# Kernel optimization log

Hardware: AMD Instinct MI355X
Metric: run time of the kernel (lower is better)

Reference implementation:

```python
import jax, jax.numpy as jnp
import numpy as np

B, IN_DIM = 1024, 128
MBD_IN, MBD_OUT, MBD_K = 64, 50, 5
BN_EPS = 1e-5


def setup_inputs() -> dict:
    key = jax.random.key(0)
    ks = jax.random.split(key, 16)
    n = lambda k, s: jax.random.normal(k, s, dtype=jnp.float32)
    return {
        "x": n(ks[0], (B, IN_DIM)),
        # MLP: 128->256->128(BN)->64, LeakyReLU(0.2)
        "W1": n(ks[1], (IN_DIM, 256)) * 0.05, "b1": jnp.zeros((256,), jnp.float32),
        "W2": n(ks[2], (256, 128)) * 0.05, "b2": jnp.zeros((128,), jnp.float32),
        "gamma": jnp.ones((128,), jnp.float32), "beta": jnp.zeros((128,), jnp.float32),
        "W3": n(ks[3], (128, 64)) * 0.05, "b3": jnp.zeros((64,), jnp.float32),
        # SelfAttention1D(64, heads=1) on a length-1 token: softmax over a single
        # key is identically 1, so output = residual + out_proj(value_proj(h)).
        # Wq/Wk provably do not affect the output and are omitted.
        "Wv": n(ks[4], (64, 64)) * 0.05, "bv": jnp.zeros((64,), jnp.float32),
        "Wo": n(ks[5], (64, 64)) * 0.05, "bo": jnp.zeros((64,), jnp.float32),
        # MinibatchDiscrimination tensor T: [64, 50, 5], init 0.05*randn as in source
        "T": n(ks[6], (MBD_IN, MBD_OUT, MBD_K)) * 0.05,
        "Ws": n(ks[7], (MBD_IN + MBD_OUT, 1)) * 0.05, "bs": jnp.zeros((1,), jnp.float32),
    }


def _lrelu(h):
    return jnp.where(h > 0, h, 0.2 * h)


def reference(x, W1, b1, W2, b2, gamma, beta, W3, b3, Wv, bv, Wo, bo, T, Ws, bs):
    # --- MLP backbone (BatchNorm1d in training mode: batch statistics) ---
    h = _lrelu(x @ W1 + b1)                      # [B,256]
    h = h @ W2 + b2                              # [B,128]
    mu = h.mean(axis=0)
    var = ((h - mu) ** 2).mean(axis=0)           # biased variance (torch BN)
    h = (h - mu) * jax.lax.rsqrt(var + BN_EPS) * gamma + beta
    h = _lrelu(h)
    h = _lrelu(h @ W3 + b3)                      # [B,64]
    # --- SelfAttention1D, seq_len=1 -> attn weights == 1 ---
    h = h + (h @ Wv + bv) @ Wo + bo              # [B,64]
    # --- Minibatch discrimination: fused all-pairs L1 + exp-sum ---
    M = (h @ T.reshape(MBD_IN, MBD_OUT * MBD_K)).reshape(-1, MBD_OUT, MBD_K)  # [B,50,5]
    diff = jnp.abs(M[:, None, :, :] - M[None, :, :, :]).sum(-1)               # [B,B,50]
    o = jnp.exp(-diff).sum(axis=0) - 1.0          # [B,50] (self term exp(0)=1 removed)
    feat = jnp.concatenate([h, o], axis=1)        # [B,114]
    score = (feat @ Ws + bs).squeeze(-1)          # [B]
    return score
```

## Files before the change

kernel.cpp:

```cpp
#include <hip/hip_runtime.h>
#include <math.h>

#define LRELU(v) ((v) > 0.f ? (v) : 0.2f * (v))


__global__ __launch_bounds__(256) void k1_mlp12(
    const float* __restrict__ x,
    const float* __restrict__ W1, const float* __restrict__ b1,
    const float* __restrict__ W2, const float* __restrict__ b2,
    float* __restrict__ h2g, float* __restrict__ stats)
{
    __shared__ float xs[256];
    __shared__ float h1s[512];
    __shared__ float ssum[256];
    __shared__ float ssq[256];
    const int t = threadIdx.x;
    const int r0 = blockIdx.x * 2;

    xs[t] = x[r0 * 128 + t];
    __syncthreads();
    {
        float a0 = b1[t], a1 = a0;
        for (int k = 0; k < 128; ++k) {
            float w = W1[k * 256 + t];
            a0 += xs[k] * w;
            a1 += xs[128 + k] * w;
        }
        h1s[t] = LRELU(a0);
        h1s[256 + t] = LRELU(a1);
    }
    __syncthreads();
    {
        const int c = t & 127;
        const int rr = t >> 7;
        float a = b2[c];
        for (int k = 0; k < 256; ++k)
            a += h1s[rr * 256 + k] * W2[k * 128 + c];
        h2g[(r0 + rr) * 128 + c] = a;
        ssum[t] = a;
        ssq[t] = a * a;
    }
    __syncthreads();
    if (t < 128)      atomicAdd(stats + t, ssum[t] + ssum[128 + t]);
    else { int c = t - 128; atomicAdd(stats + 128 + c, ssq[c] + ssq[128 + c]); }
}

__global__ __launch_bounds__(256) void k2_bn_attn_m(
    const float* __restrict__ h2g, const float* __restrict__ stats,
    const float* __restrict__ gamma, const float* __restrict__ beta,
    const float* __restrict__ W3, const float* __restrict__ b3,
    const float* __restrict__ Wv, const float* __restrict__ bv,
    const float* __restrict__ Wo, const float* __restrict__ bo,
    const float* __restrict__ T2,
    float* __restrict__ h4g, float* __restrict__ Mt)
{
    __shared__ float a[256];
    __shared__ float h3s[128];
    __shared__ float vss[128];
    __shared__ float h4s[128];
    const int t = threadIdx.x;
    const int r0 = blockIdx.x * 2;
    {
        const int c = t & 127;
        float s = stats[c], ss = stats[128 + c];
        float mean = s * (1.f / 1024.f);
        float var = ss * (1.f / 1024.f) - mean * mean;
        float rstd = rsqrtf(var + 1e-5f);
        float v = (h2g[r0 * 128 + t] - mean) * rstd * gamma[c] + beta[c];
        a[t] = LRELU(v);
    }
    __syncthreads();
    const int row = t >> 6, col = t & 63;
    if (t < 128) {
        float acc = b3[col];
        for (int k = 0; k < 128; ++k) acc += a[row * 128 + k] * W3[k * 64 + col];
        h3s[row * 64 + col] = LRELU(acc);
    }
    __syncthreads();
    if (t < 128) {
        float acc = bv[col];
        for (int k = 0; k < 64; ++k) acc += h3s[row * 64 + k] * Wv[k * 64 + col];
        vss[row * 64 + col] = acc;
    }
    __syncthreads();
    if (t < 128) {
        float acc = bo[col];
        for (int k = 0; k < 64; ++k) acc += vss[row * 64 + k] * Wo[k * 64 + col];
        float h4 = h3s[row * 64 + col] + acc;
        h4s[row * 64 + col] = h4;
        h4g[(r0 + row) * 64 + col] = h4;
    }
    __syncthreads();
    if (t < 250) {
        float m0 = 0.f, m1 = 0.f;
        for (int k = 0; k < 64; ++k) {
            float w = T2[k * 250 + t];
            m0 += h4s[k] * w;
            m1 += h4s[64 + k] * w;
        }
        Mt[(size_t)t * 1024 + r0]     = m0;
        Mt[(size_t)t * 1024 + r0 + 1] = m1;
    } else {
        Mt[(size_t)t * 1024 + r0]     = 0.f;
        Mt[(size_t)t * 1024 + r0 + 1] = 0.f;
    }
    if (t < 4) {
        Mt[(size_t)(256 + t) * 1024 + r0]     = 0.f;
        Mt[(size_t)(256 + t) * 1024 + r0 + 1] = 0.f;
    }
}

__global__ __launch_bounds__(256) void k3_pairs(
    const float* __restrict__ Mt, float* __restrict__ opart)
{
    __shared__ float mi[2560];
    const int t = threadIdx.x;
    const int b = blockIdx.x;
    const int jt = b / 104;
    const int rem = b - jt * 104;
    const int ct = rem >> 3;
    const int ic = rem & 7;
    const int jl = t & 63, cl = t >> 6;
    const int j = jt * 64 + jl;
    const int c = ct * 4 + cl;
    const int i0 = ic * 128;

    for (int qq = 0; qq < 10; ++qq) {
        int idx = qq * 256 + t;
        int cc = idx >> 7, il = idx & 127;
        mi[idx] = Mt[(size_t)(ct * 20 + cc) * 1024 + i0 + il];
    }
    float mj0 = Mt[(size_t)(c * 5 + 0) * 1024 + j];
    float mj1 = Mt[(size_t)(c * 5 + 1) * 1024 + j];
    float mj2 = Mt[(size_t)(c * 5 + 2) * 1024 + j];
    float mj3 = Mt[(size_t)(c * 5 + 3) * 1024 + j];
    float mj4 = Mt[(size_t)(c * 5 + 4) * 1024 + j];
    __syncthreads();

    const float4* m0 = (const float4*)(mi + (cl * 5 + 0) * 128);
    const float4* m1 = (const float4*)(mi + (cl * 5 + 1) * 128);
    const float4* m2 = (const float4*)(mi + (cl * 5 + 2) * 128);
    const float4* m3 = (const float4*)(mi + (cl * 5 + 3) * 128);
    const float4* m4 = (const float4*)(mi + (cl * 5 + 4) * 128);

    float acc0 = 0.f, acc1 = 0.f, acc2 = 0.f, acc3 = 0.f;
    for (int q = 0; q < 32; ++q) {
        float4 v0 = m0[q], v1 = m1[q], v2 = m2[q], v3 = m3[q], v4 = m4[q];
        float d0 = fabsf(v0.x - mj0) + fabsf(v1.x - mj1) + fabsf(v2.x - mj2)
                 + fabsf(v3.x - mj3) + fabsf(v4.x - mj4);
        float d1 = fabsf(v0.y - mj0) + fabsf(v1.y - mj1) + fabsf(v2.y - mj2)
                 + fabsf(v3.y - mj3) + fabsf(v4.y - mj4);
        float d2 = fabsf(v0.z - mj0) + fabsf(v1.z - mj1) + fabsf(v2.z - mj2)
                 + fabsf(v3.z - mj3) + fabsf(v4.z - mj4);
        float d3 = fabsf(v0.w - mj0) + fabsf(v1.w - mj1) + fabsf(v2.w - mj2)
                 + fabsf(v3.w - mj3) + fabsf(v4.w - mj4);
        acc0 += __expf(-d0);
        acc1 += __expf(-d1);
        acc2 += __expf(-d2);
        acc3 += __expf(-d3);
    }
    opart[(size_t)(ic * 1024 + j) * 52 + c] = (acc0 + acc1) + (acc2 + acc3);
}

__global__ __launch_bounds__(64) void k4_score(
    const float* __restrict__ h4g, const float* __restrict__ opart,
    const float* __restrict__ Ws, const float* __restrict__ bs,
    float* __restrict__ out)
{
    const int j = blockIdx.x, t = threadIdx.x;
    float contrib = h4g[j * 64 + t] * Ws[t];
    if (t < 50) {
        float s = 0.f;
        for (int ic = 0; ic < 8; ++ic)
            s += opart[(size_t)(ic * 1024 + j) * 52 + t];
        contrib += (s - 1.0f) * Ws[64 + t];
    }
    for (int off = 32; off > 0; off >>= 1)
        contrib += __shfl_down(contrib, off, 64);
    if (t == 0) out[j] = contrib + bs[0];
}

extern "C" void kernel_launch(void* const* d_in, const int* in_sizes, int n_in,
                              void* d_out, int out_size, void* d_ws, size_t ws_size,
                              hipStream_t stream)
{
    const float* x     = (const float*)d_in[0];
    const float* W1    = (const float*)d_in[1];
    const float* b1    = (const float*)d_in[2];
    const float* W2    = (const float*)d_in[3];
    const float* b2    = (const float*)d_in[4];
    const float* gamma = (const float*)d_in[5];
    const float* beta  = (const float*)d_in[6];
    const float* W3    = (const float*)d_in[7];
    const float* b3    = (const float*)d_in[8];
    const float* Wv    = (const float*)d_in[9];
    const float* bv    = (const float*)d_in[10];
    const float* Wo    = (const float*)d_in[11];
    const float* bo    = (const float*)d_in[12];
    const float* T2    = (const float*)d_in[13];
    const float* Ws    = (const float*)d_in[14];
    const float* bs    = (const float*)d_in[15];

    float* ws    = (float*)d_ws;
    float* h2    = ws + 0;
    float* stats = ws + 131072;
    float* h4    = ws + 131328;
    float* Mt    = ws + 196864;
    float* opart = ws + 463104;
    float* out   = (float*)d_out;

    hipMemsetAsync(stats, 0, 256 * sizeof(float), stream);
    hipLaunchKernelGGL(k1_mlp12, dim3(512), dim3(256), 0, stream,
                       x, W1, b1, W2, b2, h2, stats);
    hipLaunchKernelGGL(k2_bn_attn_m, dim3(512), dim3(256), 0, stream,
                       h2, stats, gamma, beta, W3, b3, Wv, bv, Wo, bo, T2, h4, Mt);
    hipLaunchKernelGGL(k3_pairs, dim3(1664), dim3(256), 0, stream, Mt, opart);
    hipLaunchKernelGGL(k4_score, dim3(1024), dim3(64), 0, stream,
                       h4, opart, Ws, bs, out);
}
```

Baseline: 143.3 us.

## Split-K the small MLP matmuls across 512 threads and prescale M by log2e

The first two kernels now run 512 threads per block. Each dot product in the MLP and attention projections is split along K into partial sums, which are reduced in shared memory, so each thread's serial accumulation chain is shorter. M is prescaled by log2(e) so the pairwise kernel can call exp2f instead of __expf. The cost is extra shared-memory traffic and more barriers in the small kernels. The prescale also slightly changes rounding in the L1 distances.

```diff
diff --git a/kernel.cpp b/kernel.cpp
--- a/kernel.cpp
+++ b/kernel.cpp
@@ -4,7 +4,7 @@
 #define LRELU(v) ((v) > 0.f ? (v) : 0.2f * (v))
 
 
-__global__ __launch_bounds__(256) void k1_mlp12(
+__global__ __launch_bounds__(512) void k1_mlp12(
     const float* __restrict__ x,
     const float* __restrict__ W1, const float* __restrict__ b1,
     const float* __restrict__ W2, const float* __restrict__ b2,
@@ -12,40 +12,46 @@
 {
     __shared__ float xs[256];
     __shared__ float h1s[512];
+    __shared__ float hp[512];
     __shared__ float ssum[256];
     __shared__ float ssq[256];
     const int t = threadIdx.x;
     const int r0 = blockIdx.x * 2;
 
-    xs[t] = x[r0 * 128 + t];
-    __syncthreads();
-    {
-        float a0 = b1[t], a1 = a0;
-        for (int k = 0; k < 128; ++k) {
-            float w = W1[k * 256 + t];
-            a0 += xs[k] * w;
-            a1 += xs[128 + k] * w;
-        }
-        h1s[t] = LRELU(a0);
-        h1s[256 + t] = LRELU(a1);
-    }
-    __syncthreads();
-    {
-        const int c = t & 127;
-        const int rr = t >> 7;
-        float a = b2[c];
-        for (int k = 0; k < 256; ++k)
-            a += h1s[rr * 256 + k] * W2[k * 128 + c];
-        h2g[(r0 + rr) * 128 + c] = a;
-        ssum[t] = a;
-        ssq[t] = a * a;
+    if (t < 256) xs[t] = x[r0 * 128 + t];
+    __syncthreads();
+    {
+        const int col = t & 255, row = t >> 8;
+        const float* xr = xs + row * 128;
+        float a0 = b1[col];
+        for (int k = 0; k < 128; ++k)
+            a0 += xr[k] * W1[k * 256 + col];
+        h1s[row * 256 + col] = LRELU(a0);
+    }
+    __syncthreads();
+    {
+        const int c = t & 127, rr = (t >> 7) & 1, kh = t >> 8;
+        const float* h1r = h1s + rr * 256 + kh * 128;
+        const float* w2 = W2 + kh * 128 * 128;
+        float p = 0.f;
+        for (int k = 0; k < 128; ++k)
+            p += h1r[k] * w2[k * 128 + c];
+        hp[t] = p;
+    }
+    __syncthreads();
+    if (t < 256) {
+        const int c = t & 127, rr = t >> 7;
+        float v = hp[rr * 128 + c] + hp[256 + rr * 128 + c] + b2[c];
+        h2g[(r0 + rr) * 128 + c] = v;
+        ssum[t] = v;
+        ssq[t] = v * v;
     }
     __syncthreads();
     if (t < 128)      atomicAdd(stats + t, ssum[t] + ssum[128 + t]);
-    else { int c = t - 128; atomicAdd(stats + 128 + c, ssq[c] + ssq[128 + c]); }
-}
-
-__global__ __launch_bounds__(256) void k2_bn_attn_m(
+    else if (t < 256) { int c = t - 128; atomicAdd(stats + 128 + c, ssq[c] + ssq[128 + c]); }
+}
+
+__global__ __launch_bounds__(512) void k2_bn_attn_m(
     const float* __restrict__ h2g, const float* __restrict__ stats,
     const float* __restrict__ gamma, const float* __restrict__ beta,
     const float* __restrict__ W3, const float* __restrict__ b3,
@@ -55,12 +61,14 @@
     float* __restrict__ h4g, float* __restrict__ Mt)
 {
     __shared__ float a[256];
+    __shared__ float hp[512];
     __shared__ float h3s[128];
     __shared__ float vss[128];
     __shared__ float h4s[128];
     const int t = threadIdx.x;
     const int r0 = blockIdx.x * 2;
-    {
+
+    if (t < 256) {
         const int c = t & 127;
         float s = stats[c], ss = stats[128 + c];
         float mean = s * (1.f / 1024.f);
@@ -70,43 +78,59 @@
         a[t] = LRELU(v);
     }
     __syncthreads();
-    const int row = t >> 6, col = t & 63;
+    const int col = t & 63, row = (t >> 6) & 1, kq = t >> 7;
+    {
+        const float* ar = a + row * 128 + kq * 32;
+        float p = 0.f;
+        for (int k = 0; k < 32; ++k)
+            p += ar[k] * W3[(kq * 32 + k) * 64 + col];
+        hp[t] = p;
+    }
+    __syncthreads();
     if (t < 128) {
-        float acc = b3[col];
-        for (int k = 0; k < 128; ++k) acc += a[row * 128 + k] * W3[k * 64 + col];
-        h3s[row * 64 + col] = LRELU(acc);
+        const int cc = t & 63, rr = t >> 6, o = rr * 64 + cc;
+        h3s[o] = LRELU(hp[o] + hp[128 + o] + hp[256 + o] + hp[384 + o] + b3[cc]);
+    }
+    __syncthreads();
+    {
+        const float* hr = h3s + row * 64 + kq * 16;
+        float p = 0.f;
+        for (int k = 0; k < 16; ++k)
+            p += hr[k] * Wv[(kq * 16 + k) * 64 + col];
+        hp[t] = p;
     }
     __syncthreads();
     if (t < 128) {
-        float acc = bv[col];
-        for (int k = 0; k < 64; ++k) acc += h3s[row * 64 + k] * Wv[k * 64 + col];
-        vss[row * 64 + col] = acc;
+        const int cc = t & 63, rr = t >> 6, o = rr * 64 + cc;
+        vss[o] = hp[o] + hp[128 + o] + hp[256 + o] + hp[384 + o] + bv[cc];
+    }
+    __syncthreads();
+    {
+        const float* vr = vss + row * 64 + kq * 16;
+        float p = 0.f;
+        for (int k = 0; k < 16; ++k)
+            p += vr[k] * Wo[(kq * 16 + k) * 64 + col];
+        hp[t] = p;
     }
     __syncthreads();
     if (t < 128) {
-        float acc = bo[col];
-        for (int k = 0; k < 64; ++k) acc += vss[row * 64 + k] * Wo[k * 64 + col];
-        float h4 = h3s[row * 64 + col] + acc;
-        h4s[row * 64 + col] = h4;
-        h4g[(r0 + row) * 64 + col] = h4;
-    }
-    __syncthreads();
-    if (t < 250) {
-        float m0 = 0.f, m1 = 0.f;
-        for (int k = 0; k < 64; ++k) {
-            float w = T2[k * 250 + t];
-            m0 += h4s[k] * w;
-            m1 += h4s[64 + k] * w;
-        }
-        Mt[(size_t)t * 1024 + r0]     = m0;
-        Mt[(size_t)t * 1024 + r0 + 1] = m1;
-    } else {
-        Mt[(size_t)t * 1024 + r0]     = 0.f;
-        Mt[(size_t)t * 1024 + r0 + 1] = 0.f;
-    }
-    if (t < 4) {
-        Mt[(size_t)(256 + t) * 1024 + r0]     = 0.f;
-        Mt[(size_t)(256 + t) * 1024 + r0 + 1] = 0.f;
+        const int cc = t & 63, rr = t >> 6, o = rr * 64 + cc;
+        float h4 = h3s[o] + hp[o] + hp[128 + o] + hp[256 + o] + hp[384 + o] + bo[cc];
+        h4s[o] = h4;
+        h4g[(r0 + rr) * 64 + cc] = h4;
+    }
+    __syncthreads();
+    const float LOG2E = 1.44269504088896340736f;
+    if (t < 500) {
+        const int rr = t / 250, c = t - rr * 250;
+        float m = 0.f;
+        for (int k = 0; k < 64; ++k)
+            m += h4s[rr * 64 + k] * T2[k * 250 + c];
+        Mt[(size_t)c * 1024 + r0 + rr] = m * LOG2E;
+    } else if (t < 520) {
+        const int idx = t - 500;
+        const int c = 250 + (idx >> 1), rr = idx & 1;
+        Mt[(size_t)c * 1024 + r0 + rr] = 0.f;
     }
 }
 
@@ -154,10 +178,10 @@
                  + fabsf(v3.z - mj3) + fabsf(v4.z - mj4);
         float d3 = fabsf(v0.w - mj0) + fabsf(v1.w - mj1) + fabsf(v2.w - mj2)
                  + fabsf(v3.w - mj3) + fabsf(v4.w - mj4);
-        acc0 += __expf(-d0);
-        acc1 += __expf(-d1);
-        acc2 += __expf(-d2);
-        acc3 += __expf(-d3);
+        acc0 += exp2f(-d0);
+        acc1 += exp2f(-d1);
+        acc2 += exp2f(-d2);
+        acc3 += exp2f(-d3);
     }
     opart[(size_t)(ic * 1024 + j) * 52 + c] = (acc0 + acc1) + (acc2 + acc3);
 }
@@ -210,9 +234,9 @@
     float* out   = (float*)d_out;
 
     hipMemsetAsync(stats, 0, 256 * sizeof(float), stream);
-    hipLaunchKernelGGL(k1_mlp12, dim3(512), dim3(256), 0, stream,
+    hipLaunchKernelGGL(k1_mlp12, dim3(512), dim3(512), 0, stream,
                        x, W1, b1, W2, b2, h2, stats);
-    hipLaunchKernelGGL(k2_bn_attn_m, dim3(512), dim3(256), 0, stream,
+    hipLaunchKernelGGL(k2_bn_attn_m, dim3(512), dim3(512), 0, stream,
                        h2, stats, gamma, beta, W3, b3, Wv, bv, Wo, bo, T2, h4, Mt);
     hipLaunchKernelGGL(k3_pairs, dim3(1664), dim3(256), 0, stream, Mt, opart);
     hipLaunchKernelGGL(k4_score, dim3(1024), dim3(64), 0, stream,
```

Result: no change. 145.0 us (+1.2%).
